# Performance work log

Hardware: AMD Instinct MI355X
Metric: run time of the kernel (lower is better)

## Reference

```python
import jax, jax.numpy as jnp
import numpy as np

NUM_CLASSES = 20
IOU_T = 0.5
NEG_RATIO = 3.0
VXY = 0.1
VWH = 0.2
EPS16 = 9.765625e-4  # torch.finfo(torch.float16).eps


def ltrb2xywh(b):
    return jnp.concatenate([(b[..., :2] + b[..., 2:]) * 0.5, b[..., 2:] - b[..., :2]], -1)


def xywh2ltrb(b):
    return jnp.concatenate([b[..., :2] - b[..., 2:] * 0.5, b[..., :2] + b[..., 2:] * 0.5], -1)


def pairwise_iou(gb, ab):
    # gb [G,4] ltrb, ab [A,4] ltrb -> [G,A]
    lt = jnp.maximum(gb[:, None, :2], ab[None, :, :2])
    rb = jnp.minimum(gb[:, None, 2:], ab[None, :, 2:])
    wh = jnp.clip(rb - lt, 0.0)
    inter = wh[..., 0] * wh[..., 1]
    area_g = (gb[:, 2] - gb[:, 0]) * (gb[:, 3] - gb[:, 1])
    area_a = (ab[:, 2] - ab[:, 0]) * (ab[:, 3] - ab[:, 1])
    return inter / jnp.clip(area_g[:, None] + area_a[None, :] - inter, 1e-8)


def setup_inputs() -> dict:
    key = jax.random.key(0)
    k = jax.random.split(key, 7)
    B, A, G, C = 64, 8732, 50, NUM_CLASSES + 1
    preg = jax.random.normal(k[0], (B, 4, A), jnp.float32) * 0.1
    pcls = jax.random.normal(k[1], (B, C, A), jnp.float32)
    acxy = jax.random.uniform(k[2], (A, 2), jnp.float32)
    awh = jax.random.uniform(k[3], (A, 2), jnp.float32, 0.05, 0.5)
    ancs_xywh = jnp.concatenate([acxy, awh], -1)
    gcxy = jax.random.uniform(k[4], (B, G, 2), jnp.float32, 0.2, 0.8)
    gwh = jax.random.uniform(k[5], (B, G, 2), jnp.float32, 0.05, 0.4)
    gboxes_ltrb = jnp.concatenate([gcxy - gwh * 0.5, gcxy + gwh * 0.5], -1)
    glabels = jax.random.randint(k[6], (B, G), 0, C)  # 0 == padding/background
    return {"preg": preg, "pcls": pcls, "ancs_xywh": ancs_xywh,
            "gboxes_ltrb": gboxes_ltrb, "glabels": glabels}


def _loss(preg, pcls, ancs_xywh, gboxes_ltrb, glabels):
    B, _, A = preg.shape
    preg_bad = jnp.transpose(preg, (0, 2, 1))  # [B,A,4]
    anc_ltrb = xywh2ltrb(ancs_xywh)

    def match(gb, gl):
        iou = pairwise_iou(gb, anc_ltrb)                    # [G,A]
        iou = jnp.where((gl > 0)[:, None], iou, -1.0)       # mask padded gts
        return jnp.argmax(iou, 0), jnp.max(iou, 0) >= IOU_T  # best gt per anchor, pos mask

    boxes_index, mask_pos = jax.vmap(match)(gboxes_ltrb, glabels)  # [B,A],[B,A]

    glabel = jnp.where(mask_pos, jnp.take_along_axis(glabels, boxes_index, 1), 0)  # [B,A]
    gbox_ltrb = jnp.take_along_axis(gboxes_ltrb, boxes_index[..., None], 1)        # [B,A,4]

    gxywh = ltrb2xywh(gbox_ltrb)
    txy = (gxywh[..., :2] - ancs_xywh[None, :, :2]) / (ancs_xywh[None, :, 2:] * VXY)
    twh = jnp.log(jnp.clip(gxywh[..., 2:], 1e-6) / ancs_xywh[None, :, 2:]) / VWH
    gtxywh = jnp.concatenate([txy, twh], -1)
    d = preg_bad - gtxywh
    ad = jnp.abs(d)
    sl1 = jnp.where(ad < 1.0, 0.5 * d * d, ad - 0.5).sum(-1)   # [B,A]
    posf = mask_pos.astype(preg.dtype)
    n_pos_total = jnp.clip(posf.sum(), 1.0)
    l_box = (sl1 * posf).sum() / n_pos_total

    # ---- classification: CE + OHEM hard negatives ----
    logp = jax.nn.log_softmax(pcls, axis=1)                     # [B,C,A]
    ce = -jnp.take_along_axis(logp, glabel[:, None, :], 1)[:, 0, :]  # [B,A]
    nums_pos = jnp.clip(posf.sum(-1), EPS16)                    # [B]

    loss_neg = jnp.where(mask_pos, 0.0, ce)
    order = jnp.argsort(-loss_neg, axis=-1)
    rank = jnp.argsort(order, axis=-1)
    mask_neg = (rank < (NEG_RATIO * nums_pos)[:, None]) & (~mask_pos)
    negf = mask_neg.astype(preg.dtype)

    l_conf_pos = ((ce * posf).sum(-1) / nums_pos).mean()
    l_conf_neg = ((ce * negf).sum(-1) / nums_pos).mean()
    return l_box + l_conf_pos + l_conf_neg


def reference(preg, pcls, ancs_xywh, gboxes_ltrb, glabels):
    return _loss(preg, pcls, ancs_xywh, gboxes_ltrb, glabels)
```

## Files before the change

kernel.cpp:

```cpp
#include <hip/hip_runtime.h>

#define B_ 64
#define A_ 8732
#define G_ 50
#define C_ 21
#define NBLK1 18
#define NV 35

__global__ __launch_bounds__(256) void k_match_ce(
    const float* __restrict__ preg,
    const float* __restrict__ pcls,
    const float* __restrict__ ancs,
    const float* __restrict__ gbox,
    const int*   __restrict__ glab,
    float* __restrict__ loss_neg,
    int*   __restrict__ pos_part,
    float* __restrict__ sl1_part,
    float* __restrict__ cep_part)
{
    __shared__ float4 sg[G_];
    __shared__ float  sa[G_];
    __shared__ int    slb[G_];
    __shared__ float  redf[8];
    __shared__ int    redi[4];
    const int b = blockIdx.y, tid = threadIdx.x;
    const int wid = tid >> 6, lane = tid & 63;
    const int pr_i  = blockIdx.x * 256 + tid;
    const bool valid = (pr_i * 2) < A_;
    const int a0 = (valid ? pr_i : (A_ / 2 - 1)) * 2;

    if (tid < G_) {
        float4 gp = ((const float4*)gbox)[b * G_ + tid];
        const int lb = glab[b * G_ + tid];
        slb[tid] = lb;
        if (lb <= 0) gp = make_float4(1e18f, 1e18f, 1e18f, 1e18f);
        sg[tid] = gp;
        sa[tid] = (gp.z - gp.x) * (gp.w - gp.y);
    }
    __syncthreads();

    const float4 ap0 = ((const float4*)ancs)[a0];
    const float4 ap1 = ((const float4*)ancs)[a0 + 1];
    const float al0 = ap0.x - ap0.z * 0.5f, at0 = ap0.y - ap0.w * 0.5f;
    const float ar0 = ap0.x + ap0.z * 0.5f, ab0 = ap0.y + ap0.w * 0.5f;
    const float al1 = ap1.x - ap1.z * 0.5f, at1 = ap1.y - ap1.w * 0.5f;
    const float ar1 = ap1.x + ap1.z * 0.5f, ab1 = ap1.y + ap1.w * 0.5f;
    const float area0 = (ar0 - al0) * (ab0 - at0);
    const float area1 = (ar1 - al1) * (ab1 - at1);

    float bin0 = -1.0f, bun0 = 1.0f, bin1 = -1.0f, bun1 = 1.0f;
    int bgi0 = 0, bgi1 = 0;
    for (int g = 0; g < G_; ++g) {
        const float4 gb4 = sg[g];
        const float ag = sa[g];
        const float ix0 = fmaxf(fminf(gb4.z, ar0) - fmaxf(gb4.x, al0), 0.0f);
        const float iy0 = fmaxf(fminf(gb4.w, ab0) - fmaxf(gb4.y, at0), 0.0f);
        const float ix1 = fmaxf(fminf(gb4.z, ar1) - fmaxf(gb4.x, al1), 0.0f);
        const float iy1 = fmaxf(fminf(gb4.w, ab1) - fmaxf(gb4.y, at1), 0.0f);
        const float in0 = ix0 * iy0, in1 = ix1 * iy1;
        const float un0 = fmaxf(ag + area0 - in0, 1e-8f);
        const float un1 = fmaxf(ag + area1 - in1, 1e-8f);
        if (in0 * bun0 > bin0 * un0) { bin0 = in0; bun0 = un0; bgi0 = g; }
        if (in1 * bun1 > bin1 * un1) { bin1 = in1; bun1 = un1; bgi1 = g; }
    }
    const bool pos0 = valid && (2.0f * bin0 >= bun0);
    const bool pos1 = valid && (2.0f * bin1 >= bun1);
    const int lab0 = pos0 ? slb[bgi0] : 0;
    const int lab1 = pos1 ? slb[bgi1] : 0;

    const float* pc = pcls + (size_t)b * C_ * A_ + a0;
    float2 xv[C_];
    #pragma unroll
    for (int c = 0; c < C_; ++c) xv[c] = *(const float2*)(pc + (size_t)c * A_);
    float s0 = 0.0f, s1 = 0.0f, xl0 = 0.0f, xl1 = 0.0f;
    #pragma unroll
    for (int c = 0; c < C_; ++c) {
        s0 += __expf(xv[c].x);
        s1 += __expf(xv[c].y);
        xl0 = (c == lab0) ? xv[c].x : xl0;
        xl1 = (c == lab1) ? xv[c].y : xl1;
    }
    const float ce0 = __logf(s0) - xl0;
    const float ce1 = __logf(s1) - xl1;

    if (valid)
        *(float2*)(loss_neg + (size_t)b * A_ + a0) =
            make_float2(pos0 ? 0.0f : ce0, pos1 ? 0.0f : ce1);

    float sl1 = 0.0f, cep = 0.0f; int pcnt = 0;
    const float* pr = preg + (size_t)b * 4 * A_ + a0;
    if (pos0) {
        const float4 g4 = sg[bgi0];
        const float gcx = (g4.x + g4.z) * 0.5f, gcy = (g4.y + g4.w) * 0.5f;
        const float t0 = (gcx - ap0.x) / (ap0.z * 0.1f);
        const float t1 = (gcy - ap0.y) / (ap0.w * 0.1f);
        const float t2 = __logf(fmaxf(g4.z - g4.x, 1e-6f) / ap0.z) * 5.0f;
        const float t3 = __logf(fmaxf(g4.w - g4.y, 1e-6f) / ap0.w) * 5.0f;
        #pragma unroll
        for (int k = 0; k < 4; ++k) {
            const float tv = (k == 0) ? t0 : (k == 1) ? t1 : (k == 2) ? t2 : t3;
            const float d = pr[(size_t)k * A_] - tv;
            const float ad = fabsf(d);
            sl1 += (ad < 1.0f) ? 0.5f * d * d : ad - 0.5f;
        }
        cep += ce0; ++pcnt;
    }
    if (pos1) {
        const float4 g4 = sg[bgi1];
        const float gcx = (g4.x + g4.z) * 0.5f, gcy = (g4.y + g4.w) * 0.5f;
        const float t0 = (gcx - ap1.x) / (ap1.z * 0.1f);
        const float t1 = (gcy - ap1.y) / (ap1.w * 0.1f);
        const float t2 = __logf(fmaxf(g4.z - g4.x, 1e-6f) / ap1.z) * 5.0f;
        const float t3 = __logf(fmaxf(g4.w - g4.y, 1e-6f) / ap1.w) * 5.0f;
        #pragma unroll
        for (int k = 0; k < 4; ++k) {
            const float tv = (k == 0) ? t0 : (k == 1) ? t1 : (k == 2) ? t2 : t3;
            const float d = pr[(size_t)k * A_ + 1] - tv;
            const float ad = fabsf(d);
            sl1 += (ad < 1.0f) ? 0.5f * d * d : ad - 0.5f;
        }
        cep += ce1; ++pcnt;
    }

    for (int o = 32; o > 0; o >>= 1) {
        sl1  += __shfl_down(sl1, o);
        cep  += __shfl_down(cep, o);
        pcnt += __shfl_down(pcnt, o);
    }
    if (lane == 0) { redf[wid] = sl1; redf[4 + wid] = cep; redi[wid] = pcnt; }
    __syncthreads();
    if (tid == 0) {
        const int slot = b * NBLK1 + blockIdx.x;
        pos_part[slot] = redi[0] + redi[1] + redi[2] + redi[3];
        sl1_part[slot] = redf[0] + redf[1] + redf[2] + redf[3];
        cep_part[slot] = redf[4] + redf[5] + redf[6] + redf[7];
    }
}

__global__ __launch_bounds__(256) void k_ohem(
    const float* __restrict__ loss_neg,
    const int*   __restrict__ pos_part,
    const float* __restrict__ cep_part,
    float* __restrict__ conf)
{
    __shared__ int   sred[4];
    __shared__ float sredf[4];
    __shared__ int   snp[1];
    const int b = blockIdx.x, tid = threadIdx.x;
    const int wid = tid >> 6, lane = tid & 63;

    unsigned v[NV];
    const float* src = loss_neg + (size_t)b * A_;
    #pragma unroll
    for (int i = 0; i < NV; ++i) {
        const int idx = i * 256 + tid;
        v[i] = (idx < A_) ? __float_as_uint(src[idx]) : 0u;
    }

    unsigned mx = 0u;
    #pragma unroll
    for (int i = 0; i < NV; ++i) mx = max(mx, v[i]);
    for (int o = 32; o > 0; o >>= 1)
        mx = max(mx, (unsigned)__shfl_xor((int)mx, o));
    if (lane == 0) sred[wid] = (int)mx;

    int np_l = 0; float cep_l = 0.0f;
    if (tid < NBLK1) { np_l = pos_part[b * NBLK1 + tid]; cep_l = cep_part[b * NBLK1 + tid]; }
    if (wid == 0) {
        for (int o = 32; o > 0; o >>= 1) {
            np_l  += __shfl_xor(np_l, o);
            cep_l += __shfl_xor(cep_l, o);
        }
        if (lane == 0) snp[0] = np_l;
    }
    __syncthreads();
    const unsigned mxall = max(max((unsigned)sred[0], (unsigned)sred[1]),
                               max((unsigned)sred[2], (unsigned)sred[3]));
    const int np = snp[0];
    __syncthreads();

    if (np == 0) {
        if (tid == 0) conf[b] = __uint_as_float(mxall) * 1024.0f * (1.0f / (float)B_);
        return;
    }
    const int K = min(3 * np, A_);

    unsigned thr = 0u;
    for (int bit = 30; bit >= 0; --bit) {
        const unsigned cand = thr | (1u << bit);
        if (cand > mxall) continue;
        int c = 0;
        #pragma unroll
        for (int i = 0; i < NV; ++i)
            c += __builtin_popcountll(__ballot(v[i] >= cand));
        if (lane == 0) sred[wid] = c;
        __syncthreads();
        const int tot = sred[0] + sred[1] + sred[2] + sred[3];
        __syncthreads();
        if (tot >= K) thr = cand;
    }

    float ss = 0.0f; int cgt = 0;
    #pragma unroll
    for (int i = 0; i < NV; ++i) {
        if (v[i] > thr) { ss += __uint_as_float(v[i]); ++cgt; }
    }
    for (int o = 32; o > 0; o >>= 1) {
        ss  += __shfl_xor(ss, o);
        cgt += __shfl_xor(cgt, o);
    }
    if (lane == 0) { sredf[wid] = ss; sred[wid] = cgt; }
    __syncthreads();
    if (tid == 0) {
        const float sgt = sredf[0] + sredf[1] + sredf[2] + sredf[3];
        const int   ngt = sred[0] + sred[1] + sred[2] + sred[3];
        const float t = __uint_as_float(thr);
        const float fnp = (float)np;
        const float l_neg = (sgt + (float)(K - ngt) * t) / fnp;
        const float l_pos = cep_l / fnp;
        conf[b] = (l_neg + l_pos) * (1.0f / (float)B_);
    }
}

__global__ __launch_bounds__(64) void k_final(
    const int*   __restrict__ pos_part,
    const float* __restrict__ sl1_part,
    const float* __restrict__ conf,
    float* __restrict__ out)
{
    const int lane = threadIdx.x;
    int tot = 0; float s1 = 0.0f;
    for (int j = lane; j < B_ * NBLK1; j += 64) { tot += pos_part[j]; s1 += sl1_part[j]; }
    float cf = conf[lane];
    for (int o = 32; o > 0; o >>= 1) {
        tot += __shfl_xor(tot, o);
        s1  += __shfl_xor(s1, o);
        cf  += __shfl_xor(cf, o);
    }
    if (lane == 0) out[0] = s1 / fmaxf((float)tot, 1.0f) + cf;
}

extern "C" void kernel_launch(void* const* d_in, const int* in_sizes, int n_in,
                              void* d_out, int out_size, void* d_ws, size_t ws_size,
                              hipStream_t stream)
{
    const float* preg = (const float*)d_in[0];
    const float* pcls = (const float*)d_in[1];
    const float* ancs = (const float*)d_in[2];
    const float* gbox = (const float*)d_in[3];
    const int*   glab = (const int*)d_in[4];
    float* out = (float*)d_out;

    float* loss_neg = (float*)d_ws;
    int*   pos_part = (int*)(loss_neg + (size_t)B_ * A_);
    float* sl1_part = (float*)(pos_part + B_ * NBLK1);
    float* cep_part = sl1_part + B_ * NBLK1;
    float* conf     = cep_part + B_ * NBLK1;

    dim3 g1(NBLK1, B_);
    k_match_ce<<<g1, 256, 0, stream>>>(preg, pcls, ancs, gbox, glab,
                                       loss_neg, pos_part, sl1_part, cep_part);
    k_ohem<<<B_, 256, 0, stream>>>(loss_neg, pos_part, cep_part, conf);
    k_final<<<1, 64, 0, stream>>>(pos_part, sl1_part, conf, out);
}
```

Baseline: 125.9 us.

## Split matching and cross-entropy into separate kernels with byte label handoff

Splits the fused match+CE kernel into two kernels. The matching kernel now handles 4 anchors per thread, which gives more ILP in the 50-gt IoU loop and reuses each shared-memory gt load across four anchors. It writes packed uint8 labels to workspace. A separate CE kernel reads those labels and streams pcls. This frees the CE loads from the register pressure of the matching loop, at the cost of an extra launch and a small label round-trip through memory.

Measured after the change: 133.9 us. 6.4% more time.

```diff
diff --git a/kernel.cpp b/kernel.cpp
--- a/kernel.cpp
+++ b/kernel.cpp
@@ -4,30 +4,29 @@
 #define A_ 8732
 #define G_ 50
 #define C_ 21
-#define NBLK1 18
+#define NBA 9
+#define NBB 18
 #define NV 35
 
-__global__ __launch_bounds__(256) void k_match_ce(
+__global__ __launch_bounds__(256) void k_match(
     const float* __restrict__ preg,
-    const float* __restrict__ pcls,
     const float* __restrict__ ancs,
     const float* __restrict__ gbox,
     const int*   __restrict__ glab,
-    float* __restrict__ loss_neg,
+    unsigned char* __restrict__ lab_out,
     int*   __restrict__ pos_part,
-    float* __restrict__ sl1_part,
-    float* __restrict__ cep_part)
+    float* __restrict__ sl1_part)
 {
     __shared__ float4 sg[G_];
     __shared__ float  sa[G_];
     __shared__ int    slb[G_];
-    __shared__ float  redf[8];
+    __shared__ float  redf[4];
     __shared__ int    redi[4];
     const int b = blockIdx.y, tid = threadIdx.x;
     const int wid = tid >> 6, lane = tid & 63;
-    const int pr_i  = blockIdx.x * 256 + tid;
-    const bool valid = (pr_i * 2) < A_;
-    const int a0 = (valid ? pr_i : (A_ / 2 - 1)) * 2;
+    int a0 = blockIdx.x * 1024 + tid * 4;
+    const bool valid = a0 < A_;
+    if (!valid) a0 = A_ - 4;
 
     if (tid < G_) {
         float4 gp = ((const float4*)gbox)[b * G_ + tid];
@@ -39,34 +38,89 @@
     }
     __syncthreads();
 
-    const float4 ap0 = ((const float4*)ancs)[a0];
-    const float4 ap1 = ((const float4*)ancs)[a0 + 1];
-    const float al0 = ap0.x - ap0.z * 0.5f, at0 = ap0.y - ap0.w * 0.5f;
-    const float ar0 = ap0.x + ap0.z * 0.5f, ab0 = ap0.y + ap0.w * 0.5f;
-    const float al1 = ap1.x - ap1.z * 0.5f, at1 = ap1.y - ap1.w * 0.5f;
-    const float ar1 = ap1.x + ap1.z * 0.5f, ab1 = ap1.y + ap1.w * 0.5f;
-    const float area0 = (ar0 - al0) * (ab0 - at0);
-    const float area1 = (ar1 - al1) * (ab1 - at1);
-
-    float bin0 = -1.0f, bun0 = 1.0f, bin1 = -1.0f, bun1 = 1.0f;
-    int bgi0 = 0, bgi1 = 0;
+    float4 apx[4];
+    float al[4], at[4], ar[4], ab[4], aa[4];
+    #pragma unroll
+    for (int j = 0; j < 4; ++j) {
+        const float4 ap = ((const float4*)ancs)[a0 + j];
+        apx[j] = ap;
+        al[j] = ap.x - ap.z * 0.5f; at[j] = ap.y - ap.w * 0.5f;
+        ar[j] = ap.x + ap.z * 0.5f; ab[j] = ap.y + ap.w * 0.5f;
+        aa[j] = (ar[j] - al[j]) * (ab[j] - at[j]);
+    }
+
+    float bin[4] = {-1.f, -1.f, -1.f, -1.f};
+    float bun[4] = {1.f, 1.f, 1.f, 1.f};
+    int   bgi[4] = {0, 0, 0, 0};
     for (int g = 0; g < G_; ++g) {
-        const float4 gb4 = sg[g];
-        const float ag = sa[g];
-        const float ix0 = fmaxf(fminf(gb4.z, ar0) - fmaxf(gb4.x, al0), 0.0f);
-        const float iy0 = fmaxf(fminf(gb4.w, ab0) - fmaxf(gb4.y, at0), 0.0f);
-        const float ix1 = fmaxf(fminf(gb4.z, ar1) - fmaxf(gb4.x, al1), 0.0f);
-        const float iy1 = fmaxf(fminf(gb4.w, ab1) - fmaxf(gb4.y, at1), 0.0f);
-        const float in0 = ix0 * iy0, in1 = ix1 * iy1;
-        const float un0 = fmaxf(ag + area0 - in0, 1e-8f);
-        const float un1 = fmaxf(ag + area1 - in1, 1e-8f);
-        if (in0 * bun0 > bin0 * un0) { bin0 = in0; bun0 = un0; bgi0 = g; }
-        if (in1 * bun1 > bin1 * un1) { bin1 = in1; bun1 = un1; bgi1 = g; }
-    }
-    const bool pos0 = valid && (2.0f * bin0 >= bun0);
-    const bool pos1 = valid && (2.0f * bin1 >= bun1);
-    const int lab0 = pos0 ? slb[bgi0] : 0;
-    const int lab1 = pos1 ? slb[bgi1] : 0;
+        const float4 g4 = sg[g];
+        const float  ag = sa[g];
+        #pragma unroll
+        for (int j = 0; j < 4; ++j) {
+            const float ix = fmaxf(fminf(g4.z, ar[j]) - fmaxf(g4.x, al[j]), 0.0f);
+            const float iy = fmaxf(fminf(g4.w, ab[j]) - fmaxf(g4.y, at[j]), 0.0f);
+            const float in_ = ix * iy;
+            const float un  = fmaxf(ag + aa[j] - in_, 1e-8f);
+            if (in_ * bun[j] > bin[j] * un) { bin[j] = in_; bun[j] = un; bgi[j] = g; }
+        }
+    }
+
+    unsigned lbl_pack = 0u;
+    float sl1 = 0.0f; int pcnt = 0;
+    const float* pr = preg + (size_t)b * 4 * A_ + a0;
+    #pragma unroll
+    for (int j = 0; j < 4; ++j) {
+        const bool pos = valid && (2.0f * bin[j] >= bun[j]);
+        const int lab = pos ? slb[bgi[j]] : 0;
+        lbl_pack |= ((unsigned)lab) << (8 * j);
+        if (pos) {
+            const float4 g4 = sg[bgi[j]];
+            const float4 ap = apx[j];
+            const float gcx = (g4.x + g4.z) * 0.5f, gcy = (g4.y + g4.w) * 0.5f;
+            const float t0 = (gcx - ap.x) / (ap.z * 0.1f);
+            const float t1 = (gcy - ap.y) / (ap.w * 0.1f);
+            const float t2 = __logf(fmaxf(g4.z - g4.x, 1e-6f) / ap.z) * 5.0f;
+            const float t3 = __logf(fmaxf(g4.w - g4.y, 1e-6f) / ap.w) * 5.0f;
+            #pragma unroll
+            for (int k = 0; k < 4; ++k) {
+                const float tv = (k == 0) ? t0 : (k == 1) ? t1 : (k == 2) ? t2 : t3;
+                const float d  = pr[(size_t)k * A_ + j] - tv;
+                const float ad = fabsf(d);
+                sl1 += (ad < 1.0f) ? 0.5f * d * d : ad - 0.5f;
+            }
+            ++pcnt;
+        }
+    }
+    if (valid) *(unsigned*)(lab_out + (size_t)b * A_ + a0) = lbl_pack;
+
+    for (int o = 32; o > 0; o >>= 1) {
+        sl1  += __shfl_down(sl1, o);
+        pcnt += __shfl_down(pcnt, o);
+    }
+    if (lane == 0) { redf[wid] = sl1; redi[wid] = pcnt; }
+    __syncthreads();
+    if (tid == 0) {
+        const int slot = b * NBA + blockIdx.x;
+        pos_part[slot] = redi[0] + redi[1] + redi[2] + redi[3];
+        sl1_part[slot] = redf[0] + redf[1] + redf[2] + redf[3];
+    }
+}
+
+__global__ __launch_bounds__(256) void k_ce(
+    const float* __restrict__ pcls,
+    const unsigned char* __restrict__ lab_in,
+    float* __restrict__ loss_neg,
+    float* __restrict__ cep_part)
+{
+    __shared__ float redf[4];
+    const int b = blockIdx.y, tid = threadIdx.x;
+    const int wid = tid >> 6, lane = tid & 63;
+    const int pr_i = blockIdx.x * 256 + tid;
+    const bool valid = (pr_i * 2) < A_;
+    const int a0 = (valid ? pr_i : (A_ / 2 - 1)) * 2;
+
+    const unsigned char* lp = lab_in + (size_t)b * A_ + a0;
+    const int lab0 = lp[0], lab1 = lp[1];
 
     const float* pc = pcls + (size_t)b * C_ * A_ + a0;
     float2 xv[C_];
@@ -82,59 +136,18 @@
     }
     const float ce0 = __logf(s0) - xl0;
     const float ce1 = __logf(s1) - xl1;
+    const bool pos0 = lab0 > 0, pos1 = lab1 > 0;
 
     if (valid)
         *(float2*)(loss_neg + (size_t)b * A_ + a0) =
             make_float2(pos0 ? 0.0f : ce0, pos1 ? 0.0f : ce1);
 
-    float sl1 = 0.0f, cep = 0.0f; int pcnt = 0;
-    const float* pr = preg + (size_t)b * 4 * A_ + a0;
-    if (pos0) {
-        const float4 g4 = sg[bgi0];
-        const float gcx = (g4.x + g4.z) * 0.5f, gcy = (g4.y + g4.w) * 0.5f;
-        const float t0 = (gcx - ap0.x) / (ap0.z * 0.1f);
-        const float t1 = (gcy - ap0.y) / (ap0.w * 0.1f);
-        const float t2 = __logf(fmaxf(g4.z - g4.x, 1e-6f) / ap0.z) * 5.0f;
-        const float t3 = __logf(fmaxf(g4.w - g4.y, 1e-6f) / ap0.w) * 5.0f;
-        #pragma unroll
-        for (int k = 0; k < 4; ++k) {
-            const float tv = (k == 0) ? t0 : (k == 1) ? t1 : (k == 2) ? t2 : t3;
-            const float d = pr[(size_t)k * A_] - tv;
-            const float ad = fabsf(d);
-            sl1 += (ad < 1.0f) ? 0.5f * d * d : ad - 0.5f;
-        }
-        cep += ce0; ++pcnt;
-    }
-    if (pos1) {
-        const float4 g4 = sg[bgi1];
-        const float gcx = (g4.x + g4.z) * 0.5f, gcy = (g4.y + g4.w) * 0.5f;
-        const float t0 = (gcx - ap1.x) / (ap1.z * 0.1f);
-        const float t1 = (gcy - ap1.y) / (ap1.w * 0.1f);
-        const float t2 = __logf(fmaxf(g4.z - g4.x, 1e-6f) / ap1.z) * 5.0f;
-        const float t3 = __logf(fmaxf(g4.w - g4.y, 1e-6f) / ap1.w) * 5.0f;
-        #pragma unroll
-        for (int k = 0; k < 4; ++k) {
-            const float tv = (k == 0) ? t0 : (k == 1) ? t1 : (k == 2) ? t2 : t3;
-            const float d = pr[(size_t)k * A_ + 1] - tv;
-            const float ad = fabsf(d);
-            sl1 += (ad < 1.0f) ? 0.5f * d * d : ad - 0.5f;
-        }
-        cep += ce1; ++pcnt;
-    }
-
-    for (int o = 32; o > 0; o >>= 1) {
-        sl1  += __shfl_down(sl1, o);
-        cep  += __shfl_down(cep, o);
-        pcnt += __shfl_down(pcnt, o);
-    }
-    if (lane == 0) { redf[wid] = sl1; redf[4 + wid] = cep; redi[wid] = pcnt; }
-    __syncthreads();
-    if (tid == 0) {
-        const int slot = b * NBLK1 + blockIdx.x;
-        pos_part[slot] = redi[0] + redi[1] + redi[2] + redi[3];
-        sl1_part[slot] = redf[0] + redf[1] + redf[2] + redf[3];
-        cep_part[slot] = redf[4] + redf[5] + redf[6] + redf[7];
-    }
+    float cep = valid ? ((pos0 ? ce0 : 0.0f) + (pos1 ? ce1 : 0.0f)) : 0.0f;
+    for (int o = 32; o > 0; o >>= 1) cep += __shfl_down(cep, o);
+    if (lane == 0) redf[wid] = cep;
+    __syncthreads();
+    if (tid == 0)
+        cep_part[b * NBB + blockIdx.x] = redf[0] + redf[1] + redf[2] + redf[3];
 }
 
 __global__ __launch_bounds__(256) void k_ohem(
@@ -165,7 +178,8 @@
     if (lane == 0) sred[wid] = (int)mx;
 
     int np_l = 0; float cep_l = 0.0f;
-    if (tid < NBLK1) { np_l = pos_part[b * NBLK1 + tid]; cep_l = cep_part[b * NBLK1 + tid]; }
+    if (tid < NBA) np_l = pos_part[b * NBA + tid];
+    if (tid < NBB) cep_l = cep_part[b * NBB + tid];
     if (wid == 0) {
         for (int o = 32; o > 0; o >>= 1) {
             np_l  += __shfl_xor(np_l, o);
@@ -230,7 +244,7 @@
 {
     const int lane = threadIdx.x;
     int tot = 0; float s1 = 0.0f;
-    for (int j = lane; j < B_ * NBLK1; j += 64) { tot += pos_part[j]; s1 += sl1_part[j]; }
+    for (int j = lane; j < B_ * NBA; j += 64) { tot += pos_part[j]; s1 += sl1_part[j]; }
     float cf = conf[lane];
     for (int o = 32; o > 0; o >>= 1) {
         tot += __shfl_xor(tot, o);
@@ -252,14 +266,15 @@
     float* out = (float*)d_out;
 
     float* loss_neg = (float*)d_ws;
-    int*   pos_part = (int*)(loss_neg + (size_t)B_ * A_);
-    float* sl1_part = (float*)(pos_part + B_ * NBLK1);
-    float* cep_part = sl1_part + B_ * NBLK1;
-    float* conf     = cep_part + B_ * NBLK1;
-
-    dim3 g1(NBLK1, B_);
-    k_match_ce<<<g1, 256, 0, stream>>>(preg, pcls, ancs, gbox, glab,
-                                       loss_neg, pos_part, sl1_part, cep_part);
+    unsigned char* lab_ws = (unsigned char*)(loss_neg + (size_t)B_ * A_);
+    int*   pos_part = (int*)(lab_ws + (size_t)B_ * A_);
+    float* sl1_part = (float*)(pos_part + B_ * NBA);
+    float* cep_part = sl1_part + B_ * NBA;
+    float* conf     = cep_part + B_ * NBB;
+
+    dim3 gA(NBA, B_), gB(NBB, B_);
+    k_match<<<gA, 256, 0, stream>>>(preg, ancs, gbox, glab, lab_ws, pos_part, sl1_part);
+    k_ce<<<gB, 256, 0, stream>>>(pcls, lab_ws, loss_neg, cep_part);
     k_ohem<<<B_, 256, 0, stream>>>(loss_neg, pos_part, cep_part, conf);
     k_final<<<1, 64, 0, stream>>>(pos_part, sl1_part, conf, out);
 }
```

## Drop shared GT staging, hoist pcls loads, vectorize OHEM loads as uint4

Applied to the files above, without the earlier changes.

The match kernel no longer stages GT boxes in shared memory behind a barrier. It now reads boxes and labels directly from global memory in the loop, skipping padded GTs with a branch, and issues the 21 class-logit loads before the IoU loop so their latency overlaps the matching work. The OHEM kernel loads its row of losses as 16-byte uint4 vectors and counts through four ballots per vector. This trades the shared-memory barrier for repeated global/scalar reads and per-thread divergent skips, and it drops the union clamp.

Measured after the change: 132.2 us. +5.0%, slower.

```diff
diff --git a/kernel.cpp b/kernel.cpp
--- a/kernel.cpp
+++ b/kernel.cpp
@@ -4,10 +4,11 @@
 #define A_ 8732
 #define G_ 50
 #define C_ 21
-#define NBLK1 18
-#define NV 35
-
-__global__ __launch_bounds__(256) void k_match_ce(
+#define NBF 18
+#define NQ 2183
+#define NV4 9
+
+__global__ __launch_bounds__(256) void k_fused(
     const float* __restrict__ preg,
     const float* __restrict__ pcls,
     const float* __restrict__ ancs,
@@ -18,26 +19,18 @@
     float* __restrict__ sl1_part,
     float* __restrict__ cep_part)
 {
-    __shared__ float4 sg[G_];
-    __shared__ float  sa[G_];
-    __shared__ int    slb[G_];
-    __shared__ float  redf[8];
-    __shared__ int    redi[4];
+    __shared__ float redf[8];
+    __shared__ int   redi[4];
     const int b = blockIdx.y, tid = threadIdx.x;
     const int wid = tid >> 6, lane = tid & 63;
-    const int pr_i  = blockIdx.x * 256 + tid;
-    const bool valid = (pr_i * 2) < A_;
+    const int pr_i = blockIdx.x * 256 + tid;
+    const bool valid = (2 * pr_i) < A_;
     const int a0 = (valid ? pr_i : (A_ / 2 - 1)) * 2;
 
-    if (tid < G_) {
-        float4 gp = ((const float4*)gbox)[b * G_ + tid];
-        const int lb = glab[b * G_ + tid];
-        slb[tid] = lb;
-        if (lb <= 0) gp = make_float4(1e18f, 1e18f, 1e18f, 1e18f);
-        sg[tid] = gp;
-        sa[tid] = (gp.z - gp.x) * (gp.w - gp.y);
-    }
-    __syncthreads();
+    const float* pc = pcls + b * (C_ * A_) + a0;
+    float2 xv[C_];
+    #pragma unroll
+    for (int c = 0; c < C_; ++c) xv[c] = *(const float2*)(pc + c * A_);
 
     const float4 ap0 = ((const float4*)ancs)[a0];
     const float4 ap1 = ((const float4*)ancs)[a0 + 1];
@@ -45,34 +38,37 @@
     const float ar0 = ap0.x + ap0.z * 0.5f, ab0 = ap0.y + ap0.w * 0.5f;
     const float al1 = ap1.x - ap1.z * 0.5f, at1 = ap1.y - ap1.w * 0.5f;
     const float ar1 = ap1.x + ap1.z * 0.5f, ab1 = ap1.y + ap1.w * 0.5f;
-    const float area0 = (ar0 - al0) * (ab0 - at0);
-    const float area1 = (ar1 - al1) * (ab1 - at1);
-
+    const float aa0 = (ar0 - al0) * (ab0 - at0);
+    const float aa1 = (ar1 - al1) * (ab1 - at1);
+
+    const float* gb = gbox + b * (G_ * 4);
+    const int*   gl = glab + b * G_;
     float bin0 = -1.0f, bun0 = 1.0f, bin1 = -1.0f, bun1 = 1.0f;
     int bgi0 = 0, bgi1 = 0;
     for (int g = 0; g < G_; ++g) {
-        const float4 gb4 = sg[g];
-        const float ag = sa[g];
-        const float ix0 = fmaxf(fminf(gb4.z, ar0) - fmaxf(gb4.x, al0), 0.0f);
-        const float iy0 = fmaxf(fminf(gb4.w, ab0) - fmaxf(gb4.y, at0), 0.0f);
-        const float ix1 = fmaxf(fminf(gb4.z, ar1) - fmaxf(gb4.x, al1), 0.0f);
-        const float iy1 = fmaxf(fminf(gb4.w, ab1) - fmaxf(gb4.y, at1), 0.0f);
+        const int lb = gl[g];
+        if (lb <= 0) continue;
+        const float4 g4 = *(const float4*)(gb + 4 * g);
+        const float ag = (g4.z - g4.x) * (g4.w - g4.y);
+        const float ix0 = fmaxf(fminf(g4.z, ar0) - fmaxf(g4.x, al0), 0.0f);
+        const float iy0 = fmaxf(fminf(g4.w, ab0) - fmaxf(g4.y, at0), 0.0f);
+        const float ix1 = fmaxf(fminf(g4.z, ar1) - fmaxf(g4.x, al1), 0.0f);
+        const float iy1 = fmaxf(fminf(g4.w, ab1) - fmaxf(g4.y, at1), 0.0f);
         const float in0 = ix0 * iy0, in1 = ix1 * iy1;
-        const float un0 = fmaxf(ag + area0 - in0, 1e-8f);
-        const float un1 = fmaxf(ag + area1 - in1, 1e-8f);
+        const float un0 = ag + aa0 - in0;
+        const float un1 = ag + aa1 - in1;
         if (in0 * bun0 > bin0 * un0) { bin0 = in0; bun0 = un0; bgi0 = g; }
         if (in1 * bun1 > bin1 * un1) { bin1 = in1; bun1 = un1; bgi1 = g; }
     }
     const bool pos0 = valid && (2.0f * bin0 >= bun0);
     const bool pos1 = valid && (2.0f * bin1 >= bun1);
-    const int lab0 = pos0 ? slb[bgi0] : 0;
-    const int lab1 = pos1 ? slb[bgi1] : 0;
-
-    const float* pc = pcls + (size_t)b * C_ * A_ + a0;
-    float2 xv[C_];
-    #pragma unroll
-    for (int c = 0; c < C_; ++c) xv[c] = *(const float2*)(pc + (size_t)c * A_);
-    float s0 = 0.0f, s1 = 0.0f, xl0 = 0.0f, xl1 = 0.0f;
+
+    int lab0 = 0, lab1 = 0;
+    float4 g40 = make_float4(0.f, 0.f, 1.f, 1.f), g41 = g40;
+    if (pos0) { g40 = *(const float4*)(gb + 4 * bgi0); lab0 = gl[bgi0]; }
+    if (pos1) { g41 = *(const float4*)(gb + 4 * bgi1); lab1 = gl[bgi1]; }
+
+    float s0 = 0.f, s1 = 0.f, xl0 = 0.f, xl1 = 0.f;
     #pragma unroll
     for (int c = 0; c < C_; ++c) {
         s0 += __expf(xv[c].x);
@@ -84,38 +80,36 @@
     const float ce1 = __logf(s1) - xl1;
 
     if (valid)
-        *(float2*)(loss_neg + (size_t)b * A_ + a0) =
-            make_float2(pos0 ? 0.0f : ce0, pos1 ? 0.0f : ce1);
+        *(float2*)(loss_neg + b * A_ + a0) =
+            make_float2(pos0 ? 0.f : ce0, pos1 ? 0.f : ce1);
 
     float sl1 = 0.0f, cep = 0.0f; int pcnt = 0;
-    const float* pr = preg + (size_t)b * 4 * A_ + a0;
+    const float* pr = preg + b * (4 * A_) + a0;
     if (pos0) {
-        const float4 g4 = sg[bgi0];
-        const float gcx = (g4.x + g4.z) * 0.5f, gcy = (g4.y + g4.w) * 0.5f;
+        const float gcx = (g40.x + g40.z) * 0.5f, gcy = (g40.y + g40.w) * 0.5f;
         const float t0 = (gcx - ap0.x) / (ap0.z * 0.1f);
         const float t1 = (gcy - ap0.y) / (ap0.w * 0.1f);
-        const float t2 = __logf(fmaxf(g4.z - g4.x, 1e-6f) / ap0.z) * 5.0f;
-        const float t3 = __logf(fmaxf(g4.w - g4.y, 1e-6f) / ap0.w) * 5.0f;
+        const float t2 = __logf(fmaxf(g40.z - g40.x, 1e-6f) / ap0.z) * 5.0f;
+        const float t3 = __logf(fmaxf(g40.w - g40.y, 1e-6f) / ap0.w) * 5.0f;
         #pragma unroll
         for (int k = 0; k < 4; ++k) {
             const float tv = (k == 0) ? t0 : (k == 1) ? t1 : (k == 2) ? t2 : t3;
-            const float d = pr[(size_t)k * A_] - tv;
+            const float d  = pr[k * A_] - tv;
             const float ad = fabsf(d);
             sl1 += (ad < 1.0f) ? 0.5f * d * d : ad - 0.5f;
         }
         cep += ce0; ++pcnt;
     }
     if (pos1) {
-        const float4 g4 = sg[bgi1];
-        const float gcx = (g4.x + g4.z) * 0.5f, gcy = (g4.y + g4.w) * 0.5f;
+        const float gcx = (g41.x + g41.z) * 0.5f, gcy = (g41.y + g41.w) * 0.5f;
         const float t0 = (gcx - ap1.x) / (ap1.z * 0.1f);
         const float t1 = (gcy - ap1.y) / (ap1.w * 0.1f);
-        const float t2 = __logf(fmaxf(g4.z - g4.x, 1e-6f) / ap1.z) * 5.0f;
-        const float t3 = __logf(fmaxf(g4.w - g4.y, 1e-6f) / ap1.w) * 5.0f;
+        const float t2 = __logf(fmaxf(g41.z - g41.x, 1e-6f) / ap1.z) * 5.0f;
+        const float t3 = __logf(fmaxf(g41.w - g41.y, 1e-6f) / ap1.w) * 5.0f;
         #pragma unroll
         for (int k = 0; k < 4; ++k) {
             const float tv = (k == 0) ? t0 : (k == 1) ? t1 : (k == 2) ? t2 : t3;
-            const float d = pr[(size_t)k * A_ + 1] - tv;
+            const float d  = pr[k * A_ + 1] - tv;
             const float ad = fabsf(d);
             sl1 += (ad < 1.0f) ? 0.5f * d * d : ad - 0.5f;
         }
@@ -130,7 +124,7 @@
     if (lane == 0) { redf[wid] = sl1; redf[4 + wid] = cep; redi[wid] = pcnt; }
     __syncthreads();
     if (tid == 0) {
-        const int slot = b * NBLK1 + blockIdx.x;
+        const int slot = b * NBF + blockIdx.x;
         pos_part[slot] = redi[0] + redi[1] + redi[2] + redi[3];
         sl1_part[slot] = redf[0] + redf[1] + redf[2] + redf[3];
         cep_part[slot] = redf[4] + redf[5] + redf[6] + redf[7];
@@ -149,23 +143,24 @@
     const int b = blockIdx.x, tid = threadIdx.x;
     const int wid = tid >> 6, lane = tid & 63;
 
-    unsigned v[NV];
-    const float* src = loss_neg + (size_t)b * A_;
-    #pragma unroll
-    for (int i = 0; i < NV; ++i) {
+    uint4 v[NV4];
+    const uint4* src = (const uint4*)(loss_neg + b * A_);
+    #pragma unroll
+    for (int i = 0; i < NV4; ++i) {
         const int idx = i * 256 + tid;
-        v[i] = (idx < A_) ? __float_as_uint(src[idx]) : 0u;
+        v[i] = (idx < NQ) ? src[idx] : make_uint4(0u, 0u, 0u, 0u);
     }
 
     unsigned mx = 0u;
     #pragma unroll
-    for (int i = 0; i < NV; ++i) mx = max(mx, v[i]);
+    for (int i = 0; i < NV4; ++i)
+        mx = max(mx, max(max(v[i].x, v[i].y), max(v[i].z, v[i].w)));
     for (int o = 32; o > 0; o >>= 1)
         mx = max(mx, (unsigned)__shfl_xor((int)mx, o));
     if (lane == 0) sred[wid] = (int)mx;
 
     int np_l = 0; float cep_l = 0.0f;
-    if (tid < NBLK1) { np_l = pos_part[b * NBLK1 + tid]; cep_l = cep_part[b * NBLK1 + tid]; }
+    if (tid < NBF) { np_l = pos_part[b * NBF + tid]; cep_l = cep_part[b * NBF + tid]; }
     if (wid == 0) {
         for (int o = 32; o > 0; o >>= 1) {
             np_l  += __shfl_xor(np_l, o);
@@ -191,8 +186,12 @@
         if (cand > mxall) continue;
         int c = 0;
         #pragma unroll
-        for (int i = 0; i < NV; ++i)
-            c += __builtin_popcountll(__ballot(v[i] >= cand));
+        for (int i = 0; i < NV4; ++i) {
+            c += __builtin_popcountll(__ballot(v[i].x >= cand));
+            c += __builtin_popcountll(__ballot(v[i].y >= cand));
+            c += __builtin_popcountll(__ballot(v[i].z >= cand));
+            c += __builtin_popcountll(__ballot(v[i].w >= cand));
+        }
         if (lane == 0) sred[wid] = c;
         __syncthreads();
         const int tot = sred[0] + sred[1] + sred[2] + sred[3];
@@ -202,8 +201,11 @@
 
     float ss = 0.0f; int cgt = 0;
     #pragma unroll
-    for (int i = 0; i < NV; ++i) {
-        if (v[i] > thr) { ss += __uint_as_float(v[i]); ++cgt; }
+    for (int i = 0; i < NV4; ++i) {
+        if (v[i].x > thr) { ss += __uint_as_float(v[i].x); ++cgt; }
+        if (v[i].y > thr) { ss += __uint_as_float(v[i].y); ++cgt; }
+        if (v[i].z > thr) { ss += __uint_as_float(v[i].z); ++cgt; }
+        if (v[i].w > thr) { ss += __uint_as_float(v[i].w); ++cgt; }
     }
     for (int o = 32; o > 0; o >>= 1) {
         ss  += __shfl_xor(ss, o);
@@ -230,7 +232,7 @@
 {
     const int lane = threadIdx.x;
     int tot = 0; float s1 = 0.0f;
-    for (int j = lane; j < B_ * NBLK1; j += 64) { tot += pos_part[j]; s1 += sl1_part[j]; }
+    for (int j = lane; j < B_ * NBF; j += 64) { tot += pos_part[j]; s1 += sl1_part[j]; }
     float cf = conf[lane];
     for (int o = 32; o > 0; o >>= 1) {
         tot += __shfl_xor(tot, o);
@@ -253,13 +255,13 @@
 
     float* loss_neg = (float*)d_ws;
     int*   pos_part = (int*)(loss_neg + (size_t)B_ * A_);
-    float* sl1_part = (float*)(pos_part + B_ * NBLK1);
-    float* cep_part = sl1_part + B_ * NBLK1;
-    float* conf     = cep_part + B_ * NBLK1;
-
-    dim3 g1(NBLK1, B_);
-    k_match_ce<<<g1, 256, 0, stream>>>(preg, pcls, ancs, gbox, glab,
-                                       loss_neg, pos_part, sl1_part, cep_part);
+    float* sl1_part = (float*)(pos_part + B_ * NBF);
+    float* cep_part = sl1_part + B_ * NBF;
+    float* conf     = cep_part + B_ * NBF;
+
+    dim3 gF(NBF, B_);
+    k_fused<<<gF, 256, 0, stream>>>(preg, pcls, ancs, gbox, glab,
+                                    loss_neg, pos_part, sl1_part, cep_part);
     k_ohem<<<B_, 256, 0, stream>>>(loss_neg, pos_part, cep_part, conf);
     k_final<<<1, 64, 0, stream>>>(pos_part, sl1_part, conf, out);
 }
```
